# Optimization experiments

Measured on AMD Instinct MI355X. Metric: run time of the kernel, lower is better.

Reference implementation:

```python
import jax, jax.numpy as jnp
import numpy as np

DEPTH = 5

def _path_table(depth):
    # For each leaf, ancestor internal-node index and right/left direction at each of `depth` steps.
    n_internal = 2 ** depth - 1
    n_leaves = 2 ** depth
    anc = np.zeros((n_leaves, depth), dtype=np.int32)
    is_right = np.zeros((n_leaves, depth), dtype=bool)
    for leaf in range(n_leaves):
        node = leaf + n_internal
        for d in range(depth):
            parent = (node - 1) // 2
            anc[leaf, d] = parent
            is_right[leaf, d] = (node % 2 == 0)
            node = parent
    return anc, is_right


def setup_inputs() -> dict:
    key = jax.random.key(0)
    k1, k2, k3 = jax.random.split(key, 3)
    B, F, T = 131072, 128, 20
    n_internal = 2 ** DEPTH - 1
    n_leaves = 2 ** DEPTH
    x = jax.random.normal(k1, (B, F), dtype=jnp.float32)
    split_weights = jax.random.normal(k2, (T, n_internal, F), dtype=jnp.float32) * 0.1
    split_bias = jnp.zeros((T, n_internal), dtype=jnp.float32)
    leaf_logits = jax.random.normal(k3, (T, n_leaves, 2), dtype=jnp.float32) * 0.1
    tree_weights = jnp.ones((T,), dtype=jnp.float32) / T
    # feature masks: fraction 0.7 of features active per tree
    rng = np.random.default_rng(0)
    n_feat_per_tree = max(1, int(F * 0.7))
    masks = np.zeros((T, F), dtype=np.float32)
    for t in range(T):
        idx = rng.permutation(F)[:n_feat_per_tree]
        masks[t, idx] = 1.0
    feature_masks = jnp.asarray(masks)
    return {"x": x, "split_weights": split_weights, "split_bias": split_bias,
            "leaf_logits": leaf_logits, "tree_weights": tree_weights,
            "feature_masks": feature_masks}


def reference(x, split_weights, split_bias, leaf_logits, tree_weights, feature_masks):
    T, N, F = split_weights.shape
    anc, is_right = _path_table(DEPTH)  # static numpy tables [L, DEPTH]
    # Fuse feature masking into the split weights (avoids materializing [T,B,F]).
    Wm = split_weights * feature_masks[:, None, :]           # [T,N,F]
    logits = jnp.einsum('bf,tnf->tbn', x, Wm) + split_bias[:, None, :]
    sp = jax.nn.sigmoid(logits)                              # [T,B,N], temperature = 1.0
    L = N + 1
    leaf_probs = jnp.ones(sp.shape[:2] + (L,), dtype=sp.dtype)  # [T,B,L]
    for d in range(DEPTH):  # small static loop over tree depth
        g = sp[:, :, anc[:, d]]                              # [T,B,L]
        leaf_probs = leaf_probs * jnp.where(is_right[None, None, :, d], g, 1.0 - g)
    leaf_class_probs = jax.nn.softmax(leaf_logits, axis=-1)  # [T,L,2]
    tree_out = jnp.einsum('tbl,tlc->tbc', leaf_probs, leaf_class_probs)
    w = jax.nn.softmax(tree_weights)                         # [T]
    return jnp.einsum('t,tbc->bc', w, tree_out)
```

## Files before the change

### kernel.cpp

```cpp
#include <hip/hip_runtime.h>

typedef __attribute__((ext_vector_type(8))) short bf16x8;
typedef __attribute__((ext_vector_type(4))) float floatx4;

#define T_TREES 20
#define N_NODES 32
#define F_DIM 128
#define M_TILE 128
#define S_SP 36

#define NLOG2E 1.4426950408889634f

__device__ __forceinline__ short f2bf(float f) {
    unsigned u = __float_as_uint(f);
    u += 0x7fffu + ((u >> 16) & 1u);
    return (short)(u >> 16);
}
__device__ __forceinline__ float bf2f(short h) {
    return __uint_as_float(((unsigned)(unsigned short)h) << 16);
}

__device__ __forceinline__ float sig_from_scaled(float u) {
    return __builtin_amdgcn_rcpf(1.f + __builtin_amdgcn_exp2f(u));
}

__global__ void nrf_prep(const float* __restrict__ sw, const float* __restrict__ sb,
                         const float* __restrict__ ll, const float* __restrict__ tw,
                         const float* __restrict__ fm,
                         short* __restrict__ w_all, float* __restrict__ bias_p,
                         float* __restrict__ lv0) {
    int t = blockIdx.x, slice = blockIdx.y, tid = threadIdx.x;

    const float* fmt = fm + t * F_DIM;
    const float* swt = sw + t * 31 * F_DIM;
    int idx = slice * 512 + tid;
    #pragma unroll
    for (int r = 0; r < 2; ++r, idx += 256) {
        int n = idx >> 7, f = idx & 127;
        short wb = (n < 31 && fmt[f] != 0.f) ? f2bf(swt[n * F_DIM + f]) : (short)0;
        w_all[t * (N_NODES * F_DIM) + idx] = wb;
    }

    if (slice == 0) {
        __shared__ float tws[T_TREES];
        if (tid < T_TREES) tws[tid] = tw[tid];
        __syncthreads();
        if (tid < N_NODES) {
            float m = -1e30f;
            for (int i = 0; i < T_TREES; ++i) m = fmaxf(m, bf2f(f2bf(tws[i])));
            float s = 0.f;
            for (int i = 0; i < T_TREES; ++i) s += __expf(bf2f(f2bf(tws[i])) - m);
            float wt = __expf(bf2f(f2bf(tws[t])) - m) / s;

            float bv = (tid < 31) ? bf2f(f2bf(sb[t * 31 + tid])) : 0.f;
            bias_p[t * N_NODES + tid] = bv * (-NLOG2E);
            float a  = bf2f(f2bf(ll[(t * 32 + tid) * 2 + 0]));
            float bb = bf2f(f2bf(ll[(t * 32 + tid) * 2 + 1]));
            float mx = fmaxf(a, bb);
            float e0 = __expf(a - mx), e1 = __expf(bb - mx);
            lv0[t * N_NODES + tid] = wt * e0 / (e0 + e1);
        }
    }
}

__global__ __launch_bounds__(256, 4) void nrf_main(const float* __restrict__ x,
        const short* __restrict__ w_all, const float* __restrict__ bias_p,
        const float* __restrict__ lv0, float* __restrict__ out) {
    __shared__ float sp_all[4][N_NODES * S_SP];
    __shared__ float lv_s[T_TREES * N_NODES];
    __shared__ float bias_s[T_TREES * N_NODES];

    int tid = threadIdx.x;
    int wave = tid >> 6, lane = tid & 63;
    int q = lane >> 4, c16 = lane & 15;

    for (int i = tid; i < T_TREES * N_NODES; i += 256) { lv_s[i] = lv0[i]; bias_s[i] = bias_p[i]; }

    float* spb = sp_all[wave];
    int rowBase = blockIdx.x * M_TILE + wave * 32;

    bf16x8 afrag[2][4];
    #pragma unroll
    for (int mi = 0; mi < 2; ++mi) {
        const float* xr = x + (size_t)(rowBase + mi * 16 + c16) * F_DIM;
        #pragma unroll
        for (int ks = 0; ks < 4; ++ks) {
            const float4* p = (const float4*)(xr + ks * 32 + q * 8);
            float4 f0 = p[0], f1 = p[1];
            bf16x8 v;
            v[0]=f2bf(f0.x); v[1]=f2bf(f0.y); v[2]=f2bf(f0.z); v[3]=f2bf(f0.w);
            v[4]=f2bf(f1.x); v[5]=f2bf(f1.y); v[6]=f2bf(f1.z); v[7]=f2bf(f1.w);
            afrag[mi][ks] = v;
        }
    }

    int s = lane & 15, h = lane >> 4;
    int s_node = 3 + h;
    float acc0 = 0.f, acc1 = 0.f;

    bf16x8 bpp[2][2][4];
    {
        const short* wtp = w_all;
        #pragma unroll
        for (int ni = 0; ni < 2; ++ni) {
            const short* wr = wtp + (ni * 16 + c16) * F_DIM;
            #pragma unroll
            for (int ks = 0; ks < 4; ++ks)
                bpp[0][ni][ks] = *(const bf16x8*)(wr + ks * 32 + q * 8);
        }
    }

    __syncthreads();

    #pragma unroll
    for (int t = 0; t < T_TREES; ++t) {
        const int cur = t & 1, nxt = cur ^ 1;
        if (t + 1 < T_TREES) {
            const short* wtp = w_all + (t + 1) * (N_NODES * F_DIM);
            #pragma unroll
            for (int ni = 0; ni < 2; ++ni) {
                const short* wr = wtp + (ni * 16 + c16) * F_DIM;
                #pragma unroll
                for (int ks = 0; ks < 4; ++ks)
                    bpp[nxt][ni][ks] = *(const bf16x8*)(wr + ks * 32 + q * 8);
            }
        }

        floatx4 acc[2][2];
        #pragma unroll
        for (int mi = 0; mi < 2; ++mi)
            #pragma unroll
            for (int ni = 0; ni < 2; ++ni)
                acc[mi][ni] = (floatx4){0.f,0.f,0.f,0.f};
        #pragma unroll
        for (int ks = 0; ks < 4; ++ks)
            #pragma unroll
            for (int mi = 0; mi < 2; ++mi)
                #pragma unroll
                for (int ni = 0; ni < 2; ++ni)
                    acc[mi][ni] = __builtin_amdgcn_mfma_f32_16x16x32_bf16(
                        afrag[mi][ks], bpp[cur][ni][ks], acc[mi][ni], 0, 0, 0);

        #pragma unroll
        for (int ni = 0; ni < 2; ++ni) {
            int col = ni * 16 + c16;
            float bv = bias_s[t * N_NODES + col];
            #pragma unroll
            for (int mi = 0; mi < 2; ++mi) {
                float4 v;
                v.x = sig_from_scaled(fmaf(acc[mi][ni][0], -NLOG2E, bv));
                v.y = sig_from_scaled(fmaf(acc[mi][ni][1], -NLOG2E, bv));
                v.z = sig_from_scaled(fmaf(acc[mi][ni][2], -NLOG2E, bv));
                v.w = sig_from_scaled(fmaf(acc[mi][ni][3], -NLOG2E, bv));
                *(float4*)&spb[col * S_SP + mi * 16 + q * 4] = v;
            }
        }
        float g0a = spb[s],                          g0b = spb[s + 16];
        int n1 = 1 + (h >> 1);
        float g1a = spb[n1 * S_SP + s],              g1b = spb[n1 * S_SP + s + 16];
        float g2a = spb[s_node * S_SP + s],          g2b = spb[s_node * S_SP + s + 16];
        int n3a = 2 * s_node + 1, n3b = 2 * s_node + 2;
        float g3aa = spb[n3a * S_SP + s],            g3ab = spb[n3a * S_SP + s + 16];
        float g3ba = spb[n3b * S_SP + s],            g3bb = spb[n3b * S_SP + s + 16];
        int n4 = 4 * s_node + 3;
        float g4aa = spb[n4 * S_SP + s],             g4ab = spb[n4 * S_SP + s + 16];
        float g4ba = spb[(n4+1) * S_SP + s],         g4bb = spb[(n4+1) * S_SP + s + 16];
        float g4ca = spb[(n4+2) * S_SP + s],         g4cb = spb[(n4+2) * S_SP + s + 16];
        float g4da = spb[(n4+3) * S_SP + s],         g4db = spb[(n4+3) * S_SP + s + 16];

        const float* lvt = &lv_s[t * N_NODES + h * 8];

        {
            float f0 = (h & 2) ? g0a : 1.f - g0a;
            float f1 = (h & 1) ? g1a : 1.f - g1a;
            float pre = f0 * f1;
            float p1 = pre * g2a, p0 = pre - p1;
            float q1 = p0 * g3aa, q0 = p0 - q1;
            float q3 = p1 * g3ba, q2 = p1 - q3;
            float r1 = q0 * g4aa, r0 = q0 - r1;
            float r3 = q1 * g4ba, r2 = q1 - r3;
            float r5 = q2 * g4ca, r4 = q2 - r5;
            float r7 = q3 * g4da, r6 = q3 - r7;
            acc0 += r0*lvt[0] + r1*lvt[1] + r2*lvt[2] + r3*lvt[3]
                  + r4*lvt[4] + r5*lvt[5] + r6*lvt[6] + r7*lvt[7];
        }
        {
            float f0 = (h & 2) ? g0b : 1.f - g0b;
            float f1 = (h & 1) ? g1b : 1.f - g1b;
            float pre = f0 * f1;
            float p1 = pre * g2b, p0 = pre - p1;
            float q1 = p0 * g3ab, q0 = p0 - q1;
            float q3 = p1 * g3bb, q2 = p1 - q3;
            float r1 = q0 * g4ab, r0 = q0 - r1;
            float r3 = q1 * g4bb, r2 = q1 - r3;
            float r5 = q2 * g4cb, r4 = q2 - r5;
            float r7 = q3 * g4db, r6 = q3 - r7;
            acc1 += r0*lvt[0] + r1*lvt[1] + r2*lvt[2] + r3*lvt[3]
                  + r4*lvt[4] + r5*lvt[5] + r6*lvt[6] + r7*lvt[7];
        }
    }

    acc0 += __shfl_xor(acc0, 16, 64);
    acc0 += __shfl_xor(acc0, 32, 64);
    acc1 += __shfl_xor(acc1, 16, 64);
    acc1 += __shfl_xor(acc1, 32, 64);
    if (h == 0) {
        float2 o0; o0.x = acc0; o0.y = 1.f - acc0;
        *(float2*)(out + (size_t)(rowBase + s) * 2) = o0;
        float2 o1; o1.x = acc1; o1.y = 1.f - acc1;
        *(float2*)(out + (size_t)(rowBase + 16 + s) * 2) = o1;
    }
}

extern "C" void kernel_launch(void* const* d_in, const int* in_sizes, int n_in,
                              void* d_out, int out_size, void* d_ws, size_t ws_size,
                              hipStream_t stream) {
    const float* x  = (const float*)d_in[0];
    const float* sw = (const float*)d_in[1];
    const float* sb = (const float*)d_in[2];
    const float* ll = (const float*)d_in[3];
    const float* tw = (const float*)d_in[4];
    const float* fm = (const float*)d_in[5];
    float* out = (float*)d_out;

    short* w_all  = (short*)d_ws;
    float* bias_p = (float*)((char*)d_ws + 163840);
    float* lv0    = (float*)((char*)d_ws + 166400);

    dim3 pgrid(T_TREES, 8);
    nrf_prep<<<pgrid, 256, 0, stream>>>(sw, sb, ll, tw, fm, w_all, bias_p, lv0);

    int B = in_sizes[0] / F_DIM;
    nrf_main<<<B / M_TILE, 256, 0, stream>>>(x, w_all, bias_p, lv0, out);
}
```

Before: 173.6 us.

## Stage per-tree split weights through double-buffered swizzled LDS shared by all waves

Before, each wave loaded the full per-tree weight tile from global memory into registers, so every block read each tree's weights four times. Now the block loads each tree's tile cooperatively, two vectors per thread, into a double-buffered XOR-swizzled LDS stage, and all waves read their B fragments from LDS. The next tree is prefetched into registers and written to the alternate buffer at the end of each iteration. This cuts global/L2 traffic and register pressure, but adds 16KB of LDS, which may reduce occupancy, plus a block-wide barrier every tree iteration.

Result: faster. 140.3 us, median of 2 (-19.2%).

```diff
diff --git a/kernel.cpp b/kernel.cpp
--- a/kernel.cpp
+++ b/kernel.cpp
@@ -66,6 +66,7 @@
 __global__ __launch_bounds__(256, 4) void nrf_main(const float* __restrict__ x,
         const short* __restrict__ w_all, const float* __restrict__ bias_p,
         const float* __restrict__ lv0, float* __restrict__ out) {
+    __shared__ short bstage[2][N_NODES * F_DIM];
     __shared__ float sp_all[4][N_NODES * S_SP];
     __shared__ float lv_s[T_TREES * N_NODES];
     __shared__ float bias_s[T_TREES * N_NODES];
@@ -94,35 +95,39 @@
         }
     }
 
+    const unsigned soff0 = (unsigned)(tid * 32) ^ ((unsigned)((tid >> 3) & 7) << 4);
+    const bf16x8* wsrc = (const bf16x8*)w_all + tid * 2;
+
+    {
+        bf16x8 s0 = wsrc[0], s1 = wsrc[1];
+        *(bf16x8*)((char*)bstage[0] + soff0) = s0;
+        *(bf16x8*)((char*)bstage[0] + (soff0 ^ 16u)) = s1;
+    }
+
     int s = lane & 15, h = lane >> 4;
     int s_node = 3 + h;
     float acc0 = 0.f, acc1 = 0.f;
-
-    bf16x8 bpp[2][2][4];
-    {
-        const short* wtp = w_all;
-        #pragma unroll
-        for (int ni = 0; ni < 2; ++ni) {
-            const short* wr = wtp + (ni * 16 + c16) * F_DIM;
-            #pragma unroll
-            for (int ks = 0; ks < 4; ++ks)
-                bpp[0][ni][ks] = *(const bf16x8*)(wr + ks * 32 + q * 8);
-        }
-    }
-
     __syncthreads();
 
     #pragma unroll
     for (int t = 0; t < T_TREES; ++t) {
         const int cur = t & 1, nxt = cur ^ 1;
+        bf16x8 pf0, pf1;
         if (t + 1 < T_TREES) {
-            const short* wtp = w_all + (t + 1) * (N_NODES * F_DIM);
-            #pragma unroll
-            for (int ni = 0; ni < 2; ++ni) {
-                const short* wr = wtp + (ni * 16 + c16) * F_DIM;
-                #pragma unroll
-                for (int ks = 0; ks < 4; ++ks)
-                    bpp[nxt][ni][ks] = *(const bf16x8*)(wr + ks * 32 + q * 8);
+            const bf16x8* src = (const bf16x8*)(w_all + (t + 1) * (N_NODES * F_DIM)) + tid * 2;
+            pf0 = src[0]; pf1 = src[1];
+        }
+
+        bf16x8 bfrag[2][4];
+        const char* bb = (const char*)bstage[cur];
+        #pragma unroll
+        for (int ni = 0; ni < 2; ++ni) {
+            unsigned row = (unsigned)(ni * 16 + c16);
+            unsigned swz = (row & 7u) << 4;
+            #pragma unroll
+            for (int ks = 0; ks < 4; ++ks) {
+                unsigned lin = row * 256u + (unsigned)(ks * 64 + q * 16);
+                bfrag[ni][ks] = *(const bf16x8*)(bb + (lin ^ swz));
             }
         }
 
@@ -139,7 +144,7 @@
                 #pragma unroll
                 for (int ni = 0; ni < 2; ++ni)
                     acc[mi][ni] = __builtin_amdgcn_mfma_f32_16x16x32_bf16(
-                        afrag[mi][ks], bpp[cur][ni][ks], acc[mi][ni], 0, 0, 0);
+                        afrag[mi][ks], bfrag[ni][ks], acc[mi][ni], 0, 0, 0);
 
         #pragma unroll
         for (int ni = 0; ni < 2; ++ni) {
@@ -198,6 +203,12 @@
             acc1 += r0*lvt[0] + r1*lvt[1] + r2*lvt[2] + r3*lvt[3]
                   + r4*lvt[4] + r5*lvt[5] + r6*lvt[6] + r7*lvt[7];
         }
+
+        if (t + 1 < T_TREES) {
+            *(bf16x8*)((char*)bstage[nxt] + soff0) = pf0;
+            *(bf16x8*)((char*)bstage[nxt] + (soff0 ^ 16u)) = pf1;
+        }
+        __syncthreads();
     }
 
     acc0 += __shfl_xor(acc0, 16, 64);
```
